# Kernel optimization log

Measured on AMD Instinct MI355X. Metric: run time of the kernel, lower is better.

## Reference

```python
import jax, jax.numpy as jnp
import numpy as np

H = 1024
S = 2048
B = 16

def setup_inputs() -> dict:
    key = jax.random.key(0)
    k1, k2, k3, k4, k5, k6 = jax.random.split(key, 6)
    hidden = jax.random.normal(k1, (1, B, H), dtype=jnp.float32)
    encoder_outputs = jax.random.normal(k2, (S, B, H), dtype=jnp.float32)
    seq_mask = jax.random.randint(k3, (B, S), 0, 2, dtype=jnp.int32)
    # nn.Linear(2H, H): weight [H, 2H], bias [H]
    lim1 = 1.0 / np.sqrt(2 * H)
    attn_w = jax.random.uniform(k4, (H, 2 * H), minval=-lim1, maxval=lim1, dtype=jnp.float32)
    attn_b = jax.random.uniform(k5, (H,), minval=-lim1, maxval=lim1, dtype=jnp.float32)
    # nn.Linear(H, 1, bias=False): weight [1, H]
    lim2 = 1.0 / np.sqrt(H)
    score_w = jax.random.uniform(k6, (1, H), minval=-lim2, maxval=lim2, dtype=jnp.float32)
    return {"hidden": hidden, "encoder_outputs": encoder_outputs, "seq_mask": seq_mask,
            "attn_w": attn_w, "attn_b": attn_b, "score_w": score_w}

def reference(hidden, encoder_outputs, seq_mask, attn_w, attn_b, score_w):
    # Faithful to: cat([hidden.repeat(S,1,1), encoder_outputs], -1) @ attn_w.T + attn_b
    # Split the concat-linear into two GEMMs (identical math, avoids the big concat).
    h = hidden.shape[-1]
    Wh = attn_w[:, :h]   # acts on repeated hidden
    We = attn_w[:, h:]   # acts on encoder outputs
    # hidden: [1,B,H] broadcasts over S; encoder_outputs: [S,B,H]
    pre = jnp.einsum('obh,kh->obk', hidden, Wh) + jnp.einsum('sbh,kh->sbk', encoder_outputs, We) + attn_b
    proj = jnp.tanh(pre)                               # [S,B,H]
    energies = jnp.einsum('sbh,oh->sbo', proj, score_w)[..., 0]  # [S,B]
    energies = energies.T                              # [B,S] (transpose(0,1) in original)
    energies = jnp.where(seq_mask.astype(bool), jnp.float32(-1e12), energies)
    attn = jax.nn.softmax(energies, axis=1)            # [B,S]
    return attn[:, None, :]                            # [B,1,S]
```

## Files before the change

### kernel.cpp

```cpp
#include <hip/hip_runtime.h>
#include <hip/hip_bf16.h>

#define HDIM 1024
#define SEQ 2048
#define BATCH 16
#define M_TOT (SEQ*BATCH)
#define NBLK 4
#define BM 128
#define BN 256
#define BK 32
#define NKT (HDIM/BK)

typedef __attribute__((ext_vector_type(8))) short short8;
typedef __attribute__((ext_vector_type(4))) float f32x4;

typedef const void __attribute__((address_space(1))) gvoid_t;
typedef void __attribute__((address_space(3))) svoid_t;
#define GLD16(gp, lp) __builtin_amdgcn_global_load_lds((gvoid_t*)(gp), (svoid_t*)(lp), 16, 0, 0)

static __device__ __forceinline__ unsigned short f2bf(float f) {
    unsigned int x = __float_as_uint(f);
    unsigned int r = (x + 0x7FFFu + ((x >> 16) & 1u)) >> 16;
    return (unsigned short)r;
}

__global__ __launch_bounds__(256) void qk_kernel(const float* __restrict__ hidden,
                                                 const float* __restrict__ attn_w,
                                                 const float* __restrict__ attn_b,
                                                 float* __restrict__ q) {
    int k = blockIdx.x;
    int tid = threadIdx.x;
    const float* w = attn_w + (size_t)k * (2 * HDIM);
    float p[BATCH];
#pragma unroll
    for (int b = 0; b < BATCH; b++) p[b] = 0.f;
    for (int h = tid; h < HDIM; h += 256) {
        float wv = w[h];
#pragma unroll
        for (int b = 0; b < BATCH; b++) p[b] += hidden[b * HDIM + h] * wv;
    }
#pragma unroll
    for (int b = 0; b < BATCH; b++) {
        for (int off = 32; off; off >>= 1) p[b] += __shfl_down(p[b], off);
    }
    __shared__ float red[4][BATCH];
    int lane = tid & 63, wid = tid >> 6;
    if (lane == 0) {
#pragma unroll
        for (int b = 0; b < BATCH; b++) red[wid][b] = p[b];
    }
    __syncthreads();
    if (tid < BATCH) {
        float s = red[0][tid] + red[1][tid] + red[2][tid] + red[3][tid] + attn_b[k];
        q[(size_t)tid * HDIM + k] = s;
    }
}

__global__ __launch_bounds__(256) void conv_kernel(const float* __restrict__ attn_w,
                                                   __hip_bfloat16* __restrict__ web) {
    size_t i0 = ((size_t)blockIdx.x * 256 + threadIdx.x) * 8;
    int n = (int)(i0 >> 10);
    int h = (int)(i0 & 1023);
    const float4* src = reinterpret_cast<const float4*>(attn_w + (size_t)n * (2 * HDIM) + HDIM + h);
    float4 a = src[0], b = src[1];
    union { unsigned short u[8]; short8 v; } cv;
    cv.u[0] = f2bf(a.x); cv.u[1] = f2bf(a.y); cv.u[2] = f2bf(a.z); cv.u[3] = f2bf(a.w);
    cv.u[4] = f2bf(b.x); cv.u[5] = f2bf(b.y); cv.u[6] = f2bf(b.z); cv.u[7] = f2bf(b.w);
    *reinterpret_cast<short8*>((unsigned short*)web + i0) = cv.v;
}

__global__ __launch_bounds__(256) void conv_enc(const float* __restrict__ src,
                                                __hip_bfloat16* __restrict__ dst) {
    size_t i0 = ((size_t)blockIdx.x * 256 + threadIdx.x) * 8;
    const float4* s = reinterpret_cast<const float4*>(src + i0);
    float4 a = s[0], b = s[1];
    union { unsigned short u[8]; short8 v; } cv;
    cv.u[0] = f2bf(a.x); cv.u[1] = f2bf(a.y); cv.u[2] = f2bf(a.z); cv.u[3] = f2bf(a.w);
    cv.u[4] = f2bf(b.x); cv.u[5] = f2bf(b.y); cv.u[6] = f2bf(b.z); cv.u[7] = f2bf(b.w);
    *reinterpret_cast<short8*>((unsigned short*)dst + i0) = cv.v;
}

__global__ __launch_bounds__(512, 4) void gemm_bf(const __hip_bfloat16* __restrict__ encb,
                                                  const __hip_bfloat16* __restrict__ web,
                                                  const float* __restrict__ q,
                                                  const float* __restrict__ score_w,
                                                  float* __restrict__ part) {
    __shared__ __align__(16) char pool[49152];
    __hip_bfloat16 (*As)[BM * BK] = reinterpret_cast<__hip_bfloat16 (*)[BM * BK]>(pool);
    __hip_bfloat16 (*Bs)[BN * BK] = reinterpret_cast<__hip_bfloat16 (*)[BN * BK]>(pool + 16384);
    float* q_lds = reinterpret_cast<float*>(pool);
    float* sc_lds = reinterpret_cast<float*>(pool + 16384);
    float* eng = reinterpret_cast<float*>(pool + 17408);

    int tid = threadIdx.x;
    int lane = tid & 63;
    int wid = tid >> 6;
    int wr = wid >> 2;
    int wc = wid & 3;
    int bn = blockIdx.x, bm = blockIdx.y;
    int m0 = bm * BM, n0 = bn * BN;

    int srow = tid >> 2;
    int scol = (tid & 3) * 8;
    const __hip_bfloat16* gA = encb + (size_t)(m0 + srow) * HDIM + scol;
    const __hip_bfloat16* gB0 = web + (size_t)(n0 + srow) * HDIM + scol;
    const __hip_bfloat16* gB1 = web + (size_t)(n0 + 128 + srow) * HDIM + scol;
    unsigned loA = wid * 512;
    unsigned loB0 = wid * 512;
    unsigned loB1 = 4096 + wid * 512;

    f32x4 acc[4][4];
#pragma unroll
    for (int i = 0; i < 4; i++)
#pragma unroll
        for (int j = 0; j < 4; j++) acc[i][j] = (f32x4)0.f;

    auto STAGE = [&](int buf, int kt) {
        GLD16(gA + kt * BK, &As[buf][loA]);
        GLD16(gB0 + kt * BK, &Bs[buf][loB0]);
        GLD16(gB1 + kt * BK, &Bs[buf][loB1]);
    };

    auto COMPUTE = [&](int buf) {
        short8 af[4], bfr[4];
        int rA = wr * 64 + (lane & 15);
        int rB = wc * 64 + (lane & 15);
        int ko = (lane >> 4) * 8;
#pragma unroll
        for (int i = 0; i < 4; i++) af[i] = *reinterpret_cast<const short8*>(&As[buf][(rA + i * 16) * BK + ko]);
#pragma unroll
        for (int j = 0; j < 4; j++) bfr[j] = *reinterpret_cast<const short8*>(&Bs[buf][(rB + j * 16) * BK + ko]);
#pragma unroll
        for (int i = 0; i < 4; i++)
#pragma unroll
            for (int j = 0; j < 4; j++)
                acc[i][j] = __builtin_amdgcn_mfma_f32_16x16x32_bf16(af[i], bfr[j], acc[i][j], 0, 0, 0);
    };

    STAGE(0, 0);
    __syncthreads();
    for (int kt = 0; kt < NKT; ++kt) {
        int cur = kt & 1;
        if (kt + 1 < NKT) STAGE(cur ^ 1, kt + 1);
        COMPUTE(cur);
        __syncthreads();
    }

    {
        int idx = tid * 8;
        int qb = idx >> 8;
        int kl = idx & 255;
        const float4* src = reinterpret_cast<const float4*>(q + (size_t)qb * HDIM + n0 + kl);
        float4 v0 = src[0], v1 = src[1];
        *reinterpret_cast<float4*>(&q_lds[qb * 256 + kl]) = v0;
        *reinterpret_cast<float4*>(&q_lds[qb * 256 + kl + 4]) = v1;
        if (tid < BN) sc_lds[tid] = score_w[n0 + tid];
    }
    __syncthreads();

    int c = lane & 15, cs = lane >> 4;
#pragma unroll
    for (int mi = 0; mi < 4; ++mi) {
#pragma unroll
        for (int r = 0; r < 4; ++r) {
            int b = cs * 4 + r;
            float s = 0.f;
#pragma unroll
            for (int j = 0; j < 4; ++j) {
                int kl = wc * 64 + j * 16 + c;
                float v = acc[mi][j][r] + q_lds[b * 256 + kl];
                float t = 1.f - 2.f / (__expf(2.f * v) + 1.f);
                s += sc_lds[kl] * t;
            }
            for (int off = 1; off < 16; off <<= 1) s += __shfl_xor(s, off);
            if (c == 0) eng[wc * 128 + wr * 64 + mi * 16 + b] = s;
        }
    }
    __syncthreads();
    if (tid < BM) {
        float s = eng[tid] + eng[128 + tid] + eng[256 + tid] + eng[384 + tid];
        part[(size_t)bn * M_TOT + m0 + tid] = s;
    }
}

__global__ __launch_bounds__(256) void softmax_kernel(const float* __restrict__ part,
                                                      const int* __restrict__ mask,
                                                      float* __restrict__ out) {
    int b = blockIdx.x;
    int tid = threadIdx.x;
    __shared__ float e_lds[SEQ];
    __shared__ float red[4], red2[4];
    int lane = tid & 63, wid = tid >> 6;
    float lmax = -3.4e38f;
    for (int it = 0; it < SEQ / 256; ++it) {
        int s = it * 256 + tid;
        size_t m = (size_t)s * BATCH + b;
        float e = 0.f;
#pragma unroll
        for (int c = 0; c < NBLK; c++) e += part[(size_t)c * M_TOT + m];
        if (mask[(size_t)b * SEQ + s]) e = -1e12f;
        e_lds[s] = e;
        lmax = fmaxf(lmax, e);
    }
    for (int off = 32; off; off >>= 1) lmax = fmaxf(lmax, __shfl_xor(lmax, off));
    if (lane == 0) red[wid] = lmax;
    __syncthreads();
    float gmax = fmaxf(fmaxf(red[0], red[1]), fmaxf(red[2], red[3]));
    float lsum = 0.f;
    for (int it = 0; it < SEQ / 256; ++it) {
        int s = it * 256 + tid;
        float p = __expf(e_lds[s] - gmax);
        e_lds[s] = p;
        lsum += p;
    }
    for (int off = 32; off; off >>= 1) lsum += __shfl_xor(lsum, off);
    if (lane == 0) red2[wid] = lsum;
    __syncthreads();
    float inv = 1.f / (red2[0] + red2[1] + red2[2] + red2[3]);
    for (int it = 0; it < SEQ / 256; ++it) {
        int s = it * 256 + tid;
        out[(size_t)b * SEQ + s] = e_lds[s] * inv;
    }
}

extern "C" void kernel_launch(void* const* d_in, const int* in_sizes, int n_in,
                              void* d_out, int out_size, void* d_ws, size_t ws_size,
                              hipStream_t stream) {
    const float* hidden   = (const float*)d_in[0];
    const float* enc      = (const float*)d_in[1];
    const int*   seq_mask = (const int*)d_in[2];
    const float* attn_w   = (const float*)d_in[3];
    const float* attn_b   = (const float*)d_in[4];
    const float* score_w  = (const float*)d_in[5];
    float* out = (float*)d_out;

    char* ws = (char*)d_ws;
    float* q = (float*)ws;
    __hip_bfloat16* web = (__hip_bfloat16*)(ws + 65536);
    float* part = (float*)(ws + 65536 + 2 * 1024 * 1024);
    __hip_bfloat16* encb = (__hip_bfloat16*)(ws + 65536 + 3 * 1024 * 1024);

    conv_enc<<<dim3((M_TOT * HDIM) / (8 * 256)), dim3(256), 0, stream>>>(enc, encb);
    conv_kernel<<<dim3((HDIM * HDIM) / (8 * 256)), dim3(256), 0, stream>>>(attn_w, web);
    qk_kernel<<<dim3(HDIM), dim3(256), 0, stream>>>(hidden, attn_w, attn_b, q);
    gemm_bf<<<dim3(NBLK, M_TOT / BM), dim3(512), 0, stream>>>(encb, web, q, score_w, part);
    softmax_kernel<<<dim3(BATCH), dim3(256), 0, stream>>>(part, seq_mask, out);
}
```

Measured before the change: 130.5 us.

## Rewrite bf16 GEMM with 256x256 tiles, swizzled LDS and phased pipelining

The fused GEMM+tanh+score kernel is replaced with a 256x256-tile, BK=64 version. It uses 128KB of LDS double-buffered with an XOR swizzle, and splits each k-tile into four compute phases that interleave global_load_lds staging with MFMAs under explicit vmcnt waits, barriers and setprio. Block IDs are remapped so neighbouring tiles land on the same XCD, and the epilogue is widened to 256 rows. The aim is more operand reuse per load, hidden memory latency and fewer LDS bank conflicts. The cost is higher register and LDS pressure (2 blocks/CU) and fewer blocks overall.

```diff
diff --git a/kernel.cpp b/kernel.cpp
--- a/kernel.cpp
+++ b/kernel.cpp
@@ -6,10 +6,10 @@
 #define BATCH 16
 #define M_TOT (SEQ*BATCH)
 #define NBLK 4
-#define BM 128
+#define BM 256
 #define BN 256
-#define BK 32
-#define NKT (HDIM/BK)
+#define BKT 64
+#define NT (HDIM/BKT)
 
 typedef __attribute__((ext_vector_type(8))) short short8;
 typedef __attribute__((ext_vector_type(4))) float f32x4;
@@ -17,6 +17,7 @@
 typedef const void __attribute__((address_space(1))) gvoid_t;
 typedef void __attribute__((address_space(3))) svoid_t;
 #define GLD16(gp, lp) __builtin_amdgcn_global_load_lds((gvoid_t*)(gp), (svoid_t*)(lp), 16, 0, 0)
+#define VMC(N) asm volatile("s_waitcnt vmcnt(" #N ")" ::: "memory")
 
 static __device__ __forceinline__ unsigned short f2bf(float f) {
     unsigned int x = __float_as_uint(f);
@@ -80,77 +81,120 @@
     *reinterpret_cast<short8*>((unsigned short*)dst + i0) = cv.v;
 }
 
-__global__ __launch_bounds__(512, 4) void gemm_bf(const __hip_bfloat16* __restrict__ encb,
-                                                  const __hip_bfloat16* __restrict__ web,
-                                                  const float* __restrict__ q,
-                                                  const float* __restrict__ score_w,
-                                                  float* __restrict__ part) {
-    __shared__ __align__(16) char pool[49152];
-    __hip_bfloat16 (*As)[BM * BK] = reinterpret_cast<__hip_bfloat16 (*)[BM * BK]>(pool);
-    __hip_bfloat16 (*Bs)[BN * BK] = reinterpret_cast<__hip_bfloat16 (*)[BN * BK]>(pool + 16384);
-    float* q_lds = reinterpret_cast<float*>(pool);
-    float* sc_lds = reinterpret_cast<float*>(pool + 16384);
-    float* eng = reinterpret_cast<float*>(pool + 17408);
+__global__ __launch_bounds__(512, 2) void gemm8(const __hip_bfloat16* __restrict__ encb,
+                                                const __hip_bfloat16* __restrict__ web,
+                                                const float* __restrict__ qv,
+                                                const float* __restrict__ score_w,
+                                                float* __restrict__ part) {
+    __shared__ __align__(16) char pool[131072];
 
     int tid = threadIdx.x;
     int lane = tid & 63;
     int wid = tid >> 6;
     int wr = wid >> 2;
     int wc = wid & 3;
-    int bn = blockIdx.x, bm = blockIdx.y;
+
+    int bid = blockIdx.x;
+    int lin = (bid & 7) * 64 + (bid >> 3);
+    int bm = lin >> 2;
+    int bn = lin & 3;
     int m0 = bm * BM, n0 = bn * BN;
 
-    int srow = tid >> 2;
-    int scol = (tid & 3) * 8;
-    const __hip_bfloat16* gA = encb + (size_t)(m0 + srow) * HDIM + scol;
-    const __hip_bfloat16* gB0 = web + (size_t)(n0 + srow) * HDIM + scol;
-    const __hip_bfloat16* gB1 = web + (size_t)(n0 + 128 + srow) * HDIM + scol;
-    unsigned loA = wid * 512;
-    unsigned loB0 = wid * 512;
-    unsigned loB1 = 4096 + wid * 512;
-
-    f32x4 acc[4][4];
-#pragma unroll
-    for (int i = 0; i < 4; i++)
+    int srow = tid >> 3;
+    int scolb = (((tid & 7) ^ ((tid >> 3) & 7)) << 4);
+    const char* eb = (const char*)encb;
+    const char* wb = (const char*)web;
+
+    auto STG = [&](const char* g, int ldsoff) {
+        GLD16(g + (size_t)srow * 2048 + scolb, pool + ldsoff + wid * 1024);
+        GLD16(g + (size_t)(srow + 64) * 2048 + scolb, pool + ldsoff + 8192 + wid * 1024);
+    };
+    auto APTR = [&](int kt, int h) { return eb + ((size_t)(m0 + h * 128) * HDIM + kt * BKT) * 2; };
+    auto BPTR = [&](int kt, int h) { return wb + ((size_t)(n0 + h * 128) * HDIM + kt * BKT) * 2; };
+#define ALDS(par, h) ((par) * 32768 + (h) * 16384)
+#define BLDS(par, h) (65536 + (par) * 32768 + (h) * 16384)
+
+    int lq = lane & 15, lh = lane >> 4;
+    int flip = (lane & 7) << 4;
+    int pks0 = lq * 128 + ((lh * 16) ^ flip);
+    int pks1 = lq * 128 + (((64 + lh * 16)) ^ flip);
+    int aFB = wr * 16384;
+    int bFB = 65536 + (wc >> 1) * 16384 + (wc & 1) * 8192;
+
+    f32x4 acc[8][4];
+#pragma unroll
+    for (int i = 0; i < 8; i++)
 #pragma unroll
         for (int j = 0; j < 4; j++) acc[i][j] = (f32x4)0.f;
-
-    auto STAGE = [&](int buf, int kt) {
-        GLD16(gA + kt * BK, &As[buf][loA]);
-        GLD16(gB0 + kt * BK, &Bs[buf][loB0]);
-        GLD16(gB1 + kt * BK, &Bs[buf][loB1]);
-    };
-
-    auto COMPUTE = [&](int buf) {
-        short8 af[4], bfr[4];
-        int rA = wr * 64 + (lane & 15);
-        int rB = wc * 64 + (lane & 15);
-        int ko = (lane >> 4) * 8;
-#pragma unroll
-        for (int i = 0; i < 4; i++) af[i] = *reinterpret_cast<const short8*>(&As[buf][(rA + i * 16) * BK + ko]);
-#pragma unroll
-        for (int j = 0; j < 4; j++) bfr[j] = *reinterpret_cast<const short8*>(&Bs[buf][(rB + j * 16) * BK + ko]);
-#pragma unroll
-        for (int i = 0; i < 4; i++)
-#pragma unroll
-            for (int j = 0; j < 4; j++)
-                acc[i][j] = __builtin_amdgcn_mfma_f32_16x16x32_bf16(af[i], bfr[j], acc[i][j], 0, 0, 0);
-    };
-
-    STAGE(0, 0);
-    __syncthreads();
-    for (int kt = 0; kt < NKT; ++kt) {
-        int cur = kt & 1;
-        if (kt + 1 < NKT) STAGE(cur ^ 1, kt + 1);
-        COMPUTE(cur);
-        __syncthreads();
-    }
-
+    short8 br[4][2];
+
+#define RD8(off) (*reinterpret_cast<const short8*>(pool + (off)))
+
+#define PHASE(Q, PAR, STAGE_STMT, PRE_CLOSE)                                              \
+    {                                                                                     \
+        if ((Q) == 0) {                                                                   \
+            _Pragma("unroll") for (int nj = 0; nj < 4; ++nj) {                            \
+                br[nj][0] = RD8(bFB + (PAR) * 32768 + nj * 2048 + pks0);                  \
+                br[nj][1] = RD8(bFB + (PAR) * 32768 + nj * 2048 + pks1);                  \
+            }                                                                             \
+        }                                                                                 \
+        short8 a0k0 = RD8(aFB + (PAR) * 32768 + (2 * (Q)) * 2048 + pks0);                 \
+        short8 a0k1 = RD8(aFB + (PAR) * 32768 + (2 * (Q)) * 2048 + pks1);                 \
+        short8 a1k0 = RD8(aFB + (PAR) * 32768 + (2 * (Q) + 1) * 2048 + pks0);             \
+        short8 a1k1 = RD8(aFB + (PAR) * 32768 + (2 * (Q) + 1) * 2048 + pks1);             \
+        STAGE_STMT;                                                                       \
+        __builtin_amdgcn_s_barrier();                                                     \
+        __builtin_amdgcn_s_setprio(1);                                                    \
+        _Pragma("unroll") for (int nj = 0; nj < 4; ++nj) {                                \
+            acc[2 * (Q)][nj] = __builtin_amdgcn_mfma_f32_16x16x32_bf16(a0k0, br[nj][0], acc[2 * (Q)][nj], 0, 0, 0); \
+            acc[2 * (Q)][nj] = __builtin_amdgcn_mfma_f32_16x16x32_bf16(a0k1, br[nj][1], acc[2 * (Q)][nj], 0, 0, 0); \
+            acc[2 * (Q) + 1][nj] = __builtin_amdgcn_mfma_f32_16x16x32_bf16(a1k0, br[nj][0], acc[2 * (Q) + 1][nj], 0, 0, 0); \
+            acc[2 * (Q) + 1][nj] = __builtin_amdgcn_mfma_f32_16x16x32_bf16(a1k1, br[nj][1], acc[2 * (Q) + 1][nj], 0, 0, 0); \
+        }                                                                                 \
+        __builtin_amdgcn_s_setprio(0);                                                    \
+        PRE_CLOSE;                                                                        \
+        __builtin_amdgcn_s_barrier();                                                     \
+        __builtin_amdgcn_sched_barrier(0);                                                \
+    }
+
+    STG(BPTR(0, 0), BLDS(0, 0));
+    STG(BPTR(0, 1), BLDS(0, 1));
+    STG(APTR(0, 0), ALDS(0, 0));
+    STG(APTR(0, 1), ALDS(0, 1));
+    STG(BPTR(1, 0), BLDS(1, 0));
+    STG(BPTR(1, 1), BLDS(1, 1));
+    VMC(4);
+    __builtin_amdgcn_s_barrier();
+    __builtin_amdgcn_sched_barrier(0);
+
+#pragma unroll 1
+    for (int J = 0; J < 7; ++J) {
+        int k1 = 2 * J + 1;
+        PHASE(0, 0, STG(APTR(k1, 0), ALDS(1, 0)), );
+        PHASE(1, 0, STG(APTR(k1, 1), ALDS(1, 1)), );
+        PHASE(2, 0, STG(BPTR(k1 + 1, 0), BLDS(0, 0)), );
+        PHASE(3, 0, STG(BPTR(k1 + 1, 1), BLDS(0, 1)), VMC(4));
+        PHASE(0, 1, STG(APTR(k1 + 1, 0), ALDS(0, 0)), );
+        PHASE(1, 1, STG(APTR(k1 + 1, 1), ALDS(0, 1)), );
+        PHASE(2, 1, STG(BPTR(k1 + 2, 0), BLDS(1, 0)), );
+        PHASE(3, 1, STG(BPTR(k1 + 2, 1), BLDS(1, 1)), VMC(4));
+    }
+    PHASE(0, 0, STG(APTR(15, 0), ALDS(1, 0)), );
+    PHASE(1, 0, STG(APTR(15, 1), ALDS(1, 1)), );
+    PHASE(2, 0, , );
+    PHASE(3, 0, , VMC(0));
+    PHASE(0, 1, , );
+    PHASE(1, 1, , );
+    PHASE(2, 1, , );
+    PHASE(3, 1, , );
+
+    float* q_lds = reinterpret_cast<float*>(pool);
+    float* sc_lds = reinterpret_cast<float*>(pool + 16384);
+    float* eng = reinterpret_cast<float*>(pool + 17408);
     {
-        int idx = tid * 8;
-        int qb = idx >> 8;
-        int kl = idx & 255;
-        const float4* src = reinterpret_cast<const float4*>(q + (size_t)qb * HDIM + n0 + kl);
+        int qb = tid >> 5;
+        int kl = (tid & 31) * 8;
+        const float4* src = reinterpret_cast<const float4*>(qv + (size_t)qb * HDIM + n0 + kl);
         float4 v0 = src[0], v1 = src[1];
         *reinterpret_cast<float4*>(&q_lds[qb * 256 + kl]) = v0;
         *reinterpret_cast<float4*>(&q_lds[qb * 256 + kl + 4]) = v1;
@@ -158,29 +202,32 @@
     }
     __syncthreads();
 
-    int c = lane & 15, cs = lane >> 4;
-#pragma unroll
-    for (int mi = 0; mi < 4; ++mi) {
+#pragma unroll
+    for (int mi = 0; mi < 8; ++mi) {
 #pragma unroll
         for (int r = 0; r < 4; ++r) {
-            int b = cs * 4 + r;
+            int b = lh * 4 + r;
             float s = 0.f;
 #pragma unroll
-            for (int j = 0; j < 4; ++j) {
-                int kl = wc * 64 + j * 16 + c;
-                float v = acc[mi][j][r] + q_lds[b * 256 + kl];
+            for (int nj = 0; nj < 4; ++nj) {
+                int kl = wc * 64 + nj * 16 + lq;
+                float v = acc[mi][nj][r] + q_lds[b * 256 + kl];
                 float t = 1.f - 2.f / (__expf(2.f * v) + 1.f);
                 s += sc_lds[kl] * t;
             }
             for (int off = 1; off < 16; off <<= 1) s += __shfl_xor(s, off);
-            if (c == 0) eng[wc * 128 + wr * 64 + mi * 16 + b] = s;
+            if (lq == 0) eng[wc * 256 + wr * 128 + mi * 16 + b] = s;
         }
     }
     __syncthreads();
     if (tid < BM) {
-        float s = eng[tid] + eng[128 + tid] + eng[256 + tid] + eng[384 + tid];
+        float s = eng[tid] + eng[256 + tid] + eng[512 + tid] + eng[768 + tid];
         part[(size_t)bn * M_TOT + m0 + tid] = s;
     }
+#undef PHASE
+#undef RD8
+#undef ALDS
+#undef BLDS
 }
 
 __global__ __launch_bounds__(256) void softmax_kernel(const float* __restrict__ part,
@@ -243,6 +290,6 @@
     conv_enc<<<dim3((M_TOT * HDIM) / (8 * 256)), dim3(256), 0, stream>>>(enc, encb);
     conv_kernel<<<dim3((HDIM * HDIM) / (8 * 256)), dim3(256), 0, stream>>>(attn_w, web);
     qk_kernel<<<dim3(HDIM), dim3(256), 0, stream>>>(hidden, attn_w, attn_b, q);
-    gemm_bf<<<dim3(NBLK, M_TOT / BM), dim3(512), 0, stream>>>(encb, web, q, score_w, part);
+    gemm8<<<dim3(NBLK * (M_TOT / BM)), dim3(512), 0, stream>>>(encb, web, q, score_w, part);
     softmax_kernel<<<dim3(BATCH), dim3(256), 0, stream>>>(part, seq_mask, out);
 }
```

Measured after the change: 121.7 us. 1.07x faster.
